# Performance work log

Hardware: AMD Instinct MI355X
Metric: run time of the kernel (lower is better)

The kernel has to match this reference:

```python
import jax, jax.numpy as jnp
import numpy as np

B, F, V, D_EMB = 16384, 32, 50000, 16
D_IN = F * D_EMB            # 512, concat embedding dim
N_TASK, N_SPEC, N_SH = 2, 2, 2
E = N_TASK * N_SPEC + N_SH  # 6 experts per CGC level
H1, H2 = 512, 256           # expert_params dims
T1, T2 = 128, 64            # tower dims


def setup_inputs() -> dict:
    key = jax.random.key(0)
    ks = iter(jax.random.split(key, 32))
    def w(shape, s=0.05):
        return jax.random.normal(next(ks), shape, jnp.float32) * s
    return dict(
        x_ids=jax.random.randint(next(ks), (B, F), 0, V),
        emb=w((F, V, D_EMB)),
        e1_W1=w((E, D_IN, H1)), e1_b1=jnp.zeros((E, H1), jnp.float32),
        e1_W2=w((E, H1, H2)), e1_b2=jnp.zeros((E, H2), jnp.float32),
        g1_Ws=w((N_TASK, D_IN, N_SPEC + N_SH)), g1_bs=jnp.zeros((N_TASK, N_SPEC + N_SH), jnp.float32),
        g1_Wsh=w((D_IN, E)), g1_bsh=jnp.zeros((E,), jnp.float32),
        e2_W1=w((E, H2, H1)), e2_b1=jnp.zeros((E, H1), jnp.float32),
        e2_W2=w((E, H1, H2)), e2_b2=jnp.zeros((E, H2), jnp.float32),
        g2_Ws=w((N_TASK, H2, N_SPEC + N_SH)), g2_bs=jnp.zeros((N_TASK, N_SPEC + N_SH), jnp.float32),
        tw_W1=w((N_TASK, H2, T1)), tw_b1=jnp.zeros((N_TASK, T1), jnp.float32),
        tw_W2=w((N_TASK, T1, T2)), tw_b2=jnp.zeros((N_TASK, T2), jnp.float32),
    )


def _cgc(x_list, W1, b1, W2, b2, Wg, bg, Wg_sh=None, bg_sh=None):
    # Stack expert inputs: task-t specific experts read x_list[t], shared read x_list[-1].
    X = jnp.stack([x_list[0]] * N_SPEC + [x_list[1]] * N_SPEC + [x_list[-1]] * N_SH)  # [E,B,Din]
    # Grouped two-layer expert MLP (BatchNorm is identity at eval-mode init).
    h = jax.nn.relu(jnp.einsum('ebd,edh->ebh', X, W1) + b1[:, None, :])   # [E,B,H1]
    out = jax.nn.relu(jnp.einsum('ebh,eho->ebo', h, W2) + b2[:, None, :])  # [E,B,H2]
    outs = []
    for t in range(N_TASK):
        gate = jax.nn.softmax(x_list[t] @ Wg[t] + bg[t], axis=-1)          # [B, N_SPEC+N_SH]
        sel = jnp.concatenate([out[t * N_SPEC:(t + 1) * N_SPEC], out[-N_SH:]], axis=0)
        outs.append(jnp.einsum('bk,kbo->bo', gate, sel))
    if Wg_sh is not None:  # shared gate only for levels < n_level
        gate = jax.nn.softmax(x_list[-1] @ Wg_sh + bg_sh, axis=-1)          # [B,E]
        outs.append(jnp.einsum('bk,kbo->bo', gate, out))
    return outs


def reference(x_ids, emb, e1_W1, e1_b1, e1_W2, e1_b2, g1_Ws, g1_bs, g1_Wsh, g1_bsh,
              e2_W1, e2_b1, e2_W2, e2_b2, g2_Ws, g2_bs, tw_W1, tw_b1, tw_W2, tw_b2):
    # Embedding lookup per sparse feature, then flatten (squeeze_dim=True).
    embed_x = emb[jnp.arange(F)[None, :], x_ids].reshape(B, D_IN)  # [B, 512]
    xs = [embed_x] * (N_TASK + 1)
    xs = _cgc(xs, e1_W1, e1_b1, e1_W2, e1_b2, g1_Ws, g1_bs, g1_Wsh, g1_bsh)  # level 1 -> 3 outs
    xs = _cgc(xs, e2_W1, e2_b1, e2_W2, e2_b2, g2_Ws, g2_bs)                  # level 2 -> 2 outs
    ys = []
    for t in range(N_TASK):
        h = jax.nn.relu(xs[t] @ tw_W1[t] + tw_b1[t])
        h = jax.nn.relu(h @ tw_W2[t] + tw_b2[t])
        ys.append(jax.nn.sigmoid(h))  # PredictionLayer('classification')
    return jnp.concatenate(ys, axis=1)  # [B, N_TASK*T2]
```

## Files before the change

kernel.cpp:

```cpp
#include <hip/hip_runtime.h>

typedef unsigned short u16;
typedef __attribute__((ext_vector_type(4))) unsigned short u16x4;
typedef __attribute__((ext_vector_type(8))) unsigned short u16x8;
typedef __attribute__((ext_vector_type(8))) short s16x8;
typedef __attribute__((ext_vector_type(4))) float f32x4;

#define BATCH 16384
#define NFEAT 32
#define NVOCAB 50000

__device__ __forceinline__ u16 f2bf(float f) {
    union { float f; unsigned u; } v; v.f = f;
    unsigned u = v.u;
    return (u16)((u + 0x7fffu + ((u >> 16) & 1u)) >> 16);
}
__device__ __forceinline__ float bf2f(u16 h) {
    union { unsigned u; float f; } v; v.u = ((unsigned)h) << 16;
    return v.f;
}

__device__ __forceinline__ void load_lds16(const u16* g, u16* l) {
    __builtin_amdgcn_global_load_lds(
        (const __attribute__((address_space(1))) void*)g,
        (__attribute__((address_space(3))) void*)l, 16, 0, 0);
}

struct PrepDesc { const float* src; u16* dst; int K; int N; int nz; int zbase; };
struct PrepArgs { PrepDesc d[6]; };

__global__ void prep_weights(PrepArgs args) {
    int z = blockIdx.z;
    int di = 0;
    #pragma unroll
    for (int i = 0; i < 6; i++)
        if (z >= args.d[i].zbase && z < args.d[i].zbase + args.d[i].nz) di = i;
    PrepDesc d = args.d[di];
    int zz = z - d.zbase;
    int k0 = blockIdx.x * 32, n0 = blockIdx.y * 32;
    if (k0 >= d.K || n0 >= d.N) return;
    __shared__ float tile[32][33];
    const float* src = d.src + (long)zz * d.K * d.N;
    u16* dst = d.dst + (long)zz * d.K * d.N;
    int tx = threadIdx.x & 31, ty = threadIdx.x >> 5;
    for (int r = ty; r < 32; r += 8) {
        int k = k0 + r, n = n0 + tx;
        tile[r][tx] = (k < d.K && n < d.N) ? src[(long)k * d.N + n] : 0.f;
    }
    __syncthreads();
    for (int r = ty; r < 32; r += 8) {
        int n = n0 + r, k = k0 + tx;
        if (n < d.N && k < d.K) dst[(long)n * d.K + k] = f2bf(tile[tx][r]);
    }
}

__global__ void gather_embed(const int* __restrict__ ids,
                             const float* __restrict__ emb,
                             u16* __restrict__ out) {
    int idx = blockIdx.x * 256 + threadIdx.x;
    int d4 = idx & 3;
    int f  = (idx >> 2) & 31;
    int b  = idx >> 7;
    int id = ids[b * NFEAT + f];
    const float4* p = (const float4*)(emb + ((long)f * NVOCAB + id) * 16) + d4;
    float4 v = *p;
    u16x4 o;
    o.x = f2bf(v.x); o.y = f2bf(v.y); o.z = f2bf(v.z); o.w = f2bf(v.w);
    *(u16x4*)(out + (long)b * 512 + f * 16 + d4 * 4) = o;
}

template<int ACT, typename OUT_T>
__global__ __launch_bounds__(256, 2)
void gemm_bt(const u16* __restrict__ A, const u16* __restrict__ Bt,
             const float* __restrict__ bias, OUT_T* __restrict__ C,
             int M, int N, int K,
             long a_zstride, int a_zdiv, long c_zstride, int c_row_stride) {
    __shared__ u16 sA[128 * 64];
    __shared__ u16 sB[128 * 64];
    const int z = blockIdx.z;
    const u16* Ab = A + (long)(z / a_zdiv) * a_zstride;
    const u16* Bb = Bt + (long)z * N * K;
    const int m0 = blockIdx.x * 128;
    const int n0 = blockIdx.y * 128;
    const int tid = threadIdx.x;
    const int lane = tid & 63;
    const int w = tid >> 6;
    const int wm = (w & 1) * 64;
    const int wn = (w >> 1) * 64;
    const int l16 = lane & 15;
    const int q = lane >> 4;

    const u16* gA[4];
    const u16* gB[4];
    u16* lA[4];
    u16* lB[4];
    #pragma unroll
    for (int i = 0; i < 4; i++) {
        int c = i * 256 + tid;
        int row = c >> 3;
        int lc = (c & 7) ^ (row & 7);
        gA[i] = Ab + (long)(m0 + row) * K + lc * 8;
        gB[i] = Bb + (long)(n0 + row) * K + lc * 8;
        int cb = (i * 256 + (tid & ~63)) * 8;
        lA[i] = &sA[cb];
        lB[i] = &sB[cb];
    }
    const int key = l16 & 7;

    f32x4 acc[4][4] = {};

    for (int k0 = 0; k0 < K; k0 += 64) {
        if (k0) __syncthreads();
        #pragma unroll
        for (int i = 0; i < 4; i++) load_lds16(gA[i] + k0, lA[i]);
        #pragma unroll
        for (int i = 0; i < 4; i++) load_lds16(gB[i] + k0, lB[i]);
        __syncthreads();
        #pragma unroll
        for (int kk = 0; kk < 2; kk++) {
            s16x8 af[4], bfr[4];
            #pragma unroll
            for (int i = 0; i < 4; i++) {
                int row = wm + i * 16 + l16;
                int pc = ((kk << 2) | q) ^ key;
                af[i] = *(const s16x8*)(&sA[row * 64 + pc * 8]);
            }
            #pragma unroll
            for (int i = 0; i < 4; i++) {
                int row = wn + i * 16 + l16;
                int pc = ((kk << 2) | q) ^ key;
                bfr[i] = *(const s16x8*)(&sB[row * 64 + pc * 8]);
            }
            #pragma unroll
            for (int mt = 0; mt < 4; mt++)
                #pragma unroll
                for (int nt = 0; nt < 4; nt++)
                    acc[mt][nt] = __builtin_amdgcn_mfma_f32_16x16x32_bf16(
                        bfr[nt], af[mt], acc[mt][nt], 0, 0, 0);
        }
    }

    const float* bb = bias + (long)z * N;
    OUT_T* Cp = C + (long)z * c_zstride;
    #pragma unroll
    for (int mt = 0; mt < 4; mt++) {
        int grow = m0 + wm + mt * 16 + l16;
        OUT_T* rowp = Cp + (long)grow * c_row_stride;
        #pragma unroll
        for (int nt = 0; nt < 4; nt++) {
            int gc = n0 + wn + nt * 16 + q * 4;
            if (gc >= N) continue;
            float4 bv = *(const float4*)(bb + gc);
            f32x4 v = acc[mt][nt];
            v.x += bv.x; v.y += bv.y; v.z += bv.z; v.w += bv.w;
            #pragma unroll
            for (int r = 0; r < 4; r++) {
                if (ACT == 1) v[r] = fmaxf(v[r], 0.f);
                else if (ACT == 2) v[r] = 1.f / (1.f + __expf(-v[r]));
            }
            if constexpr (sizeof(OUT_T) == 2) {
                u16x4 o;
                o.x = f2bf(v.x); o.y = f2bf(v.y); o.z = f2bf(v.z); o.w = f2bf(v.w);
                *(u16x4*)(rowp + gc) = o;
            } else {
                *(float4*)(rowp + gc) = *(float4*)&v;
            }
        }
    }
}

__global__ void gate_combine1(const u16* __restrict__ embed,
                              const u16* __restrict__ out1,
                              const float* __restrict__ g1Ws, const float* __restrict__ g1bs,
                              const float* __restrict__ gWsh, const float* __restrict__ gbsh,
                              u16* __restrict__ x1) {
    int b = blockIdx.x;
    __shared__ float sgw[14];
    int tid = threadIdx.x, w = tid >> 6, lane = tid & 63;
    if (w < 3) {
        int ng = (w == 2) ? 6 : 4;
        const float* W = (w == 2) ? gWsh : (g1Ws + w * 512 * 4);
        const u16* xr = embed + (long)b * 512;
        float lg[6] = {0, 0, 0, 0, 0, 0};
        for (int e = lane; e < 512; e += 64) {
            float xv = bf2f(xr[e]);
            #pragma unroll
            for (int g = 0; g < 6; g++)
                if (g < ng) lg[g] += xv * W[e * ng + g];
        }
        #pragma unroll
        for (int g = 0; g < 6; g++) {
            float v = lg[g];
            for (int off = 32; off > 0; off >>= 1) v += __shfl_xor(v, off);
            lg[g] = v;
        }
        if (lane == 0) {
            const float* bs = (w == 2) ? gbsh : (g1bs + w * 4);
            float mx = -1e30f;
            for (int g = 0; g < ng; g++) { lg[g] += bs[g]; mx = fmaxf(mx, lg[g]); }
            float s = 0.f, ex[6];
            for (int g = 0; g < ng; g++) { ex[g] = __expf(lg[g] - mx); s += ex[g]; }
            int base = (w == 2) ? 8 : w * 4;
            for (int g = 0; g < ng; g++) sgw[base + g] = ex[g] / s;
        }
    }
    __syncthreads();
    int j = tid;
    const u16* ob = out1 + (long)b * 256 + j;
    float o[6];
    #pragma unroll
    for (int k = 0; k < 6; k++) o[k] = bf2f(ob[(long)k * BATCH * 256]);
    float v0 = sgw[0] * o[0] + sgw[1] * o[1] + sgw[2] * o[4] + sgw[3] * o[5];
    float v1 = sgw[4] * o[2] + sgw[5] * o[3] + sgw[6] * o[4] + sgw[7] * o[5];
    float v2 = 0.f;
    #pragma unroll
    for (int k = 0; k < 6; k++) v2 += sgw[8 + k] * o[k];
    x1[((long)0 * BATCH + b) * 256 + j] = f2bf(v0);
    x1[((long)1 * BATCH + b) * 256 + j] = f2bf(v1);
    x1[((long)2 * BATCH + b) * 256 + j] = f2bf(v2);
}

__global__ void gate_combine2(const u16* __restrict__ x1,
                              const u16* __restrict__ out2,
                              const float* __restrict__ g2Ws, const float* __restrict__ g2bs,
                              u16* __restrict__ x2) {
    int b = blockIdx.x;
    __shared__ float sgw[8];
    int tid = threadIdx.x, w = tid >> 6, lane = tid & 63;
    if (w < 2) {
        const float* W = g2Ws + w * 256 * 4;
        const u16* xr = x1 + ((long)w * BATCH + b) * 256;
        float lg[4] = {0, 0, 0, 0};
        for (int e = lane; e < 256; e += 64) {
            float xv = bf2f(xr[e]);
            #pragma unroll
            for (int g = 0; g < 4; g++) lg[g] += xv * W[e * 4 + g];
        }
        #pragma unroll
        for (int g = 0; g < 4; g++) {
            float v = lg[g];
            for (int off = 32; off > 0; off >>= 1) v += __shfl_xor(v, off);
            lg[g] = v;
        }
        if (lane == 0) {
            float mx = -1e30f;
            for (int g = 0; g < 4; g++) { lg[g] += g2bs[w * 4 + g]; mx = fmaxf(mx, lg[g]); }
            float s = 0.f, ex[4];
            for (int g = 0; g < 4; g++) { ex[g] = __expf(lg[g] - mx); s += ex[g]; }
            for (int g = 0; g < 4; g++) sgw[w * 4 + g] = ex[g] / s;
        }
    }
    __syncthreads();
    int j = tid;
    const u16* ob = out2 + (long)b * 256 + j;
    float o[6];
    #pragma unroll
    for (int k = 0; k < 6; k++) o[k] = bf2f(ob[(long)k * BATCH * 256]);
    float v0 = sgw[0] * o[0] + sgw[1] * o[1] + sgw[2] * o[4] + sgw[3] * o[5];
    float v1 = sgw[4] * o[2] + sgw[5] * o[3] + sgw[6] * o[4] + sgw[7] * o[5];
    x2[((long)0 * BATCH + b) * 256 + j] = f2bf(v0);
    x2[((long)1 * BATCH + b) * 256 + j] = f2bf(v1);
}

extern "C" void kernel_launch(void* const* d_in, const int* in_sizes, int n_in,
                              void* d_out, int out_size, void* d_ws, size_t ws_size,
                              hipStream_t stream) {
    const int*   x_ids = (const int*)  d_in[0];
    const float* emb   = (const float*)d_in[1];
    const float* e1W1  = (const float*)d_in[2];
    const float* e1b1  = (const float*)d_in[3];
    const float* e1W2  = (const float*)d_in[4];
    const float* e1b2  = (const float*)d_in[5];
    const float* g1Ws  = (const float*)d_in[6];
    const float* g1bs  = (const float*)d_in[7];
    const float* g1Wsh = (const float*)d_in[8];
    const float* g1bsh = (const float*)d_in[9];
    const float* e2W1  = (const float*)d_in[10];
    const float* e2b1  = (const float*)d_in[11];
    const float* e2W2  = (const float*)d_in[12];
    const float* e2b2  = (const float*)d_in[13];
    const float* g2Ws  = (const float*)d_in[14];
    const float* g2bs  = (const float*)d_in[15];
    const float* twW1  = (const float*)d_in[16];
    const float* twb1  = (const float*)d_in[17];
    const float* twW2  = (const float*)d_in[18];
    const float* twb2  = (const float*)d_in[19];
    float* out = (float*)d_out;

    char* ws = (char*)d_ws;
    u16* embed   = (u16*)(ws + 0);
    u16* wt_e1W1 = (u16*)(ws + 16777216);
    u16* wt_e1W2 = (u16*)(ws + 19922944);
    u16* wt_e2W1 = (u16*)(ws + 21495808);
    u16* wt_e2W2 = (u16*)(ws + 23068672);
    u16* wt_twW1 = (u16*)(ws + 24641536);
    u16* wt_twW2 = (u16*)(ws + 24772608);
    u16* h_buf   = (u16*)(ws + 24805376);
    u16* o_buf   = (u16*)(ws + 125468672);
    u16* x1      = (u16*)(ws + 175800320);
    u16* x2      = (u16*)(ws + 200966144);
    u16* th      = (u16*)(ws + 217743360);

    PrepArgs pa;
    pa.d[0] = { e1W1, wt_e1W1, 512, 512, 6,  0 };
    pa.d[1] = { e1W2, wt_e1W2, 512, 256, 6,  6 };
    pa.d[2] = { e2W1, wt_e2W1, 256, 512, 6, 12 };
    pa.d[3] = { e2W2, wt_e2W2, 512, 256, 6, 18 };
    pa.d[4] = { twW1, wt_twW1, 256, 128, 2, 24 };
    pa.d[5] = { twW2, wt_twW2, 128,  64, 2, 26 };
    prep_weights<<<dim3(16, 16, 28), 256, 0, stream>>>(pa);

    gather_embed<<<dim3(BATCH * NFEAT * 4 / 256), 256, 0, stream>>>(x_ids, emb, embed);

    gemm_bt<1, u16><<<dim3(128, 4, 6), 256, 0, stream>>>(
        embed, wt_e1W1, e1b1, h_buf, BATCH, 512, 512,
        0L, 1, (long)BATCH * 512, 512);
    gemm_bt<1, u16><<<dim3(128, 2, 6), 256, 0, stream>>>(
        h_buf, wt_e1W2, e1b2, o_buf, BATCH, 256, 512,
        (long)BATCH * 512, 1, (long)BATCH * 256, 256);

    gate_combine1<<<dim3(BATCH), 256, 0, stream>>>(embed, o_buf, g1Ws, g1bs, g1Wsh, g1bsh, x1);

    gemm_bt<1, u16><<<dim3(128, 4, 6), 256, 0, stream>>>(
        x1, wt_e2W1, e2b1, h_buf, BATCH, 512, 256,
        (long)BATCH * 256, 2, (long)BATCH * 512, 512);
    gemm_bt<1, u16><<<dim3(128, 2, 6), 256, 0, stream>>>(
        h_buf, wt_e2W2, e2b2, o_buf, BATCH, 256, 512,
        (long)BATCH * 512, 1, (long)BATCH * 256, 256);

    gate_combine2<<<dim3(BATCH), 256, 0, stream>>>(x1, o_buf, g2Ws, g2bs, x2);

    gemm_bt<1, u16><<<dim3(128, 1, 2), 256, 0, stream>>>(
        x2, wt_twW1, twb1, th, BATCH, 128, 256,
        (long)BATCH * 256, 1, (long)BATCH * 128, 128);
    gemm_bt<2, float><<<dim3(128, 1, 2), 256, 0, stream>>>(
        th, wt_twW2, twb2, out, BATCH, 64, 128,
        (long)BATCH * 128, 1, 64L, 128);
}
```

Baseline: 534.1 us.

## Enlarge GEMM tiles, fuse tower MLP, and batch gate kernels over rows

Result: slower. 547.4 us (+2.5%).

```diff
diff --git a/kernel.cpp b/kernel.cpp
--- a/kernel.cpp
+++ b/kernel.cpp
@@ -69,197 +69,336 @@
     *(u16x4*)(out + (long)b * 512 + f * 16 + d4 * 4) = o;
 }
 
-template<int ACT, typename OUT_T>
-__global__ __launch_bounds__(256, 2)
-void gemm_bt(const u16* __restrict__ A, const u16* __restrict__ Bt,
-             const float* __restrict__ bias, OUT_T* __restrict__ C,
-             int M, int N, int K,
-             long a_zstride, int a_zdiv, long c_zstride, int c_row_stride) {
+struct GemmP {
+    const u16* A; const u16* Bt; const float* bias; u16* C;
+    int N, K, a_zshift, c_row_stride; long a_zstride, c_zstride;
+};
+
+__device__ __forceinline__ void gemm_impl(const GemmP p) {
     __shared__ u16 sA[128 * 64];
-    __shared__ u16 sB[128 * 64];
+    __shared__ u16 sB[256 * 64];
     const int z = blockIdx.z;
-    const u16* Ab = A + (long)(z / a_zdiv) * a_zstride;
-    const u16* Bb = Bt + (long)z * N * K;
+    const u16* Ab = p.A + (long)(z >> p.a_zshift) * p.a_zstride;
+    const u16* Bb = p.Bt + (long)z * p.N * p.K;
     const int m0 = blockIdx.x * 128;
-    const int n0 = blockIdx.y * 128;
+    const int n0 = blockIdx.y * 256;
     const int tid = threadIdx.x;
     const int lane = tid & 63;
     const int w = tid >> 6;
     const int wm = (w & 1) * 64;
-    const int wn = (w >> 1) * 64;
+    const int wn = (w >> 1) * 128;
     const int l16 = lane & 15;
     const int q = lane >> 4;
-
-    const u16* gA[4];
-    const u16* gB[4];
-    u16* lA[4];
-    u16* lB[4];
-    #pragma unroll
-    for (int i = 0; i < 4; i++) {
-        int c = i * 256 + tid;
-        int row = c >> 3;
-        int lc = (c & 7) ^ (row & 7);
-        gA[i] = Ab + (long)(m0 + row) * K + lc * 8;
-        gB[i] = Bb + (long)(n0 + row) * K + lc * 8;
-        int cb = (i * 256 + (tid & ~63)) * 8;
-        lA[i] = &sA[cb];
-        lB[i] = &sB[cb];
-    }
     const int key = l16 & 7;
-
-    f32x4 acc[4][4] = {};
+    const int K = p.K;
+
+    const int tr = tid >> 3;
+    const int lc = (tid & 7) ^ (tr & 7);
+    const u16* gA0 = Ab + (long)(m0 + tr) * K + lc * 8;
+    const u16* gB0 = Bb + (long)(n0 + tr) * K + lc * 8;
+    u16* lA0 = &sA[(tid & ~63) * 8];
+    u16* lB0 = &sB[(tid & ~63) * 8];
+
+    f32x4 acc[4][8] = {};
 
     for (int k0 = 0; k0 < K; k0 += 64) {
         if (k0) __syncthreads();
         #pragma unroll
-        for (int i = 0; i < 4; i++) load_lds16(gA[i] + k0, lA[i]);
-        #pragma unroll
-        for (int i = 0; i < 4; i++) load_lds16(gB[i] + k0, lB[i]);
+        for (int i = 0; i < 4; i++)
+            load_lds16(gA0 + (long)(32 * i) * K + k0, lA0 + i * 256 * 8);
+        #pragma unroll
+        for (int i = 0; i < 8; i++)
+            load_lds16(gB0 + (long)(32 * i) * K + k0, lB0 + i * 256 * 8);
         __syncthreads();
         #pragma unroll
         for (int kk = 0; kk < 2; kk++) {
-            s16x8 af[4], bfr[4];
+            const int pc = ((kk << 2) | q) ^ key;
+            s16x8 af[4], bf[8];
             #pragma unroll
-            for (int i = 0; i < 4; i++) {
-                int row = wm + i * 16 + l16;
-                int pc = ((kk << 2) | q) ^ key;
-                af[i] = *(const s16x8*)(&sA[row * 64 + pc * 8]);
-            }
+            for (int mt = 0; mt < 4; mt++)
+                af[mt] = *(const s16x8*)(&sA[(wm + mt * 16 + l16) * 64 + pc * 8]);
             #pragma unroll
-            for (int i = 0; i < 4; i++) {
-                int row = wn + i * 16 + l16;
-                int pc = ((kk << 2) | q) ^ key;
-                bfr[i] = *(const s16x8*)(&sB[row * 64 + pc * 8]);
-            }
+            for (int nt = 0; nt < 8; nt++)
+                bf[nt] = *(const s16x8*)(&sB[(wn + nt * 16 + l16) * 64 + pc * 8]);
             #pragma unroll
             for (int mt = 0; mt < 4; mt++)
                 #pragma unroll
-                for (int nt = 0; nt < 4; nt++)
+                for (int nt = 0; nt < 8; nt++)
                     acc[mt][nt] = __builtin_amdgcn_mfma_f32_16x16x32_bf16(
-                        bfr[nt], af[mt], acc[mt][nt], 0, 0, 0);
-        }
-    }
-
-    const float* bb = bias + (long)z * N;
-    OUT_T* Cp = C + (long)z * c_zstride;
+                        bf[nt], af[mt], acc[mt][nt], 0, 0, 0);
+        }
+    }
+
+    const float* bb = p.bias + (long)z * p.N;
+    u16* Cp = p.C + (long)z * p.c_zstride;
     #pragma unroll
     for (int mt = 0; mt < 4; mt++) {
         int grow = m0 + wm + mt * 16 + l16;
-        OUT_T* rowp = Cp + (long)grow * c_row_stride;
-        #pragma unroll
-        for (int nt = 0; nt < 4; nt++) {
+        u16* rowp = Cp + (long)grow * p.c_row_stride;
+        #pragma unroll
+        for (int nt = 0; nt < 8; nt++) {
             int gc = n0 + wn + nt * 16 + q * 4;
-            if (gc >= N) continue;
             float4 bv = *(const float4*)(bb + gc);
             f32x4 v = acc[mt][nt];
-            v.x += bv.x; v.y += bv.y; v.z += bv.z; v.w += bv.w;
+            v.x = fmaxf(v.x + bv.x, 0.f);
+            v.y = fmaxf(v.y + bv.y, 0.f);
+            v.z = fmaxf(v.z + bv.z, 0.f);
+            v.w = fmaxf(v.w + bv.w, 0.f);
+            u16x4 o;
+            o.x = f2bf(v.x); o.y = f2bf(v.y); o.z = f2bf(v.z); o.w = f2bf(v.w);
+            *(u16x4*)(rowp + gc) = o;
+        }
+    }
+}
+
+__global__ __launch_bounds__(256, 2) void gemm_l1a(GemmP p) { gemm_impl(p); }
+__global__ __launch_bounds__(256, 2) void gemm_l1b(GemmP p) { gemm_impl(p); }
+__global__ __launch_bounds__(256, 2) void gemm_l2a(GemmP p) { gemm_impl(p); }
+__global__ __launch_bounds__(256, 2) void gemm_l2b(GemmP p) { gemm_impl(p); }
+
+__global__ __launch_bounds__(256, 1)
+void tower_fused(const u16* __restrict__ x2, const u16* __restrict__ W1t,
+                 const float* __restrict__ b1, const u16* __restrict__ W2t,
+                 const float* __restrict__ b2, float* __restrict__ out) {
+    const int t = blockIdx.y, m0 = blockIdx.x * 64;
+    __shared__ u16 sX[64 * 256];
+    __shared__ u16 sW1[128 * 256];
+    __shared__ u16 sH[64 * 136];
+    __shared__ u16 sW2[64 * 128];
+    __shared__ float sB1[128];
+    __shared__ float sB2[64];
+    const int tid = threadIdx.x, lane = tid & 63, w = tid >> 6;
+    const int l16 = lane & 15, q = lane >> 4;
+
+    #pragma unroll
+    for (int i = 0; i < 8; i++) {
+        int c = i * 256 + tid, row = c >> 5, kc = c & 31;
+        int lcc = (kc & ~7) | ((kc & 7) ^ (row & 7));
+        load_lds16(x2 + ((long)t * BATCH + m0 + row) * 256 + lcc * 8,
+                   &sX[(i * 256 + (tid & ~63)) * 8]);
+    }
+    #pragma unroll
+    for (int i = 0; i < 16; i++) {
+        int c = i * 256 + tid, row = c >> 5, kc = c & 31;
+        int lcc = (kc & ~7) | ((kc & 7) ^ (row & 7));
+        load_lds16(W1t + ((long)t * 128 + row) * 256 + lcc * 8,
+                   &sW1[(i * 256 + (tid & ~63)) * 8]);
+    }
+    #pragma unroll
+    for (int i = 0; i < 4; i++) {
+        int c = i * 256 + tid, row = c >> 4, kc = c & 15;
+        int lcc = (kc & ~7) | ((kc & 7) ^ (row & 7));
+        load_lds16(W2t + ((long)t * 64 + row) * 128 + lcc * 8,
+                   &sW2[(i * 256 + (tid & ~63)) * 8]);
+    }
+    if (tid < 128) sB1[tid] = b1[t * 128 + tid];
+    if (tid < 64)  sB2[tid] = b2[t * 64 + tid];
+    __syncthreads();
+
+    f32x4 acc1[4][2] = {};
+    #pragma unroll
+    for (int kk = 0; kk < 8; kk++) {
+        int pcb = kk * 4 + q;
+        s16x8 af[4], bf[2];
+        #pragma unroll
+        for (int mt = 0; mt < 4; mt++) {
+            int row = mt * 16 + l16;
+            int sc = (pcb & ~7) | ((pcb & 7) ^ (row & 7));
+            af[mt] = *(const s16x8*)(&sX[row * 256 + sc * 8]);
+        }
+        #pragma unroll
+        for (int nt = 0; nt < 2; nt++) {
+            int row = w * 32 + nt * 16 + l16;
+            int sc = (pcb & ~7) | ((pcb & 7) ^ (row & 7));
+            bf[nt] = *(const s16x8*)(&sW1[row * 256 + sc * 8]);
+        }
+        #pragma unroll
+        for (int mt = 0; mt < 4; mt++)
             #pragma unroll
-            for (int r = 0; r < 4; r++) {
-                if (ACT == 1) v[r] = fmaxf(v[r], 0.f);
-                else if (ACT == 2) v[r] = 1.f / (1.f + __expf(-v[r]));
-            }
-            if constexpr (sizeof(OUT_T) == 2) {
-                u16x4 o;
-                o.x = f2bf(v.x); o.y = f2bf(v.y); o.z = f2bf(v.z); o.w = f2bf(v.w);
-                *(u16x4*)(rowp + gc) = o;
-            } else {
-                *(float4*)(rowp + gc) = *(float4*)&v;
-            }
-        }
-    }
-}
-
-__global__ void gate_combine1(const u16* __restrict__ embed,
-                              const u16* __restrict__ out1,
-                              const float* __restrict__ g1Ws, const float* __restrict__ g1bs,
-                              const float* __restrict__ gWsh, const float* __restrict__ gbsh,
-                              u16* __restrict__ x1) {
-    int b = blockIdx.x;
-    __shared__ float sgw[14];
-    int tid = threadIdx.x, w = tid >> 6, lane = tid & 63;
-    if (w < 3) {
-        int ng = (w == 2) ? 6 : 4;
-        const float* W = (w == 2) ? gWsh : (g1Ws + w * 512 * 4);
-        const u16* xr = embed + (long)b * 512;
-        float lg[6] = {0, 0, 0, 0, 0, 0};
-        for (int e = lane; e < 512; e += 64) {
-            float xv = bf2f(xr[e]);
+            for (int nt = 0; nt < 2; nt++)
+                acc1[mt][nt] = __builtin_amdgcn_mfma_f32_16x16x32_bf16(
+                    bf[nt], af[mt], acc1[mt][nt], 0, 0, 0);
+    }
+    #pragma unroll
+    for (int mt = 0; mt < 4; mt++) {
+        int row = mt * 16 + l16;
+        #pragma unroll
+        for (int nt = 0; nt < 2; nt++) {
+            int col = w * 32 + nt * 16 + q * 4;
+            f32x4 v = acc1[mt][nt];
+            u16x4 o;
+            o.x = f2bf(fmaxf(v.x + sB1[col + 0], 0.f));
+            o.y = f2bf(fmaxf(v.y + sB1[col + 1], 0.f));
+            o.z = f2bf(fmaxf(v.z + sB1[col + 2], 0.f));
+            o.w = f2bf(fmaxf(v.w + sB1[col + 3], 0.f));
+            *(u16x4*)(&sH[row * 136 + col]) = o;
+        }
+    }
+    __syncthreads();
+
+    f32x4 acc2[4] = {};
+    #pragma unroll
+    for (int kk = 0; kk < 4; kk++) {
+        s16x8 af[4], bf;
+        #pragma unroll
+        for (int mt = 0; mt < 4; mt++) {
+            int row = mt * 16 + l16;
+            af[mt] = *(const s16x8*)(&sH[row * 136 + kk * 32 + q * 8]);
+        }
+        {
+            int row = w * 16 + l16;
+            int pc = kk * 4 + q;
+            int sc = (pc & ~7) | ((pc & 7) ^ (row & 7));
+            bf = *(const s16x8*)(&sW2[row * 128 + sc * 8]);
+        }
+        #pragma unroll
+        for (int mt = 0; mt < 4; mt++)
+            acc2[mt] = __builtin_amdgcn_mfma_f32_16x16x32_bf16(
+                bf, af[mt], acc2[mt], 0, 0, 0);
+    }
+    #pragma unroll
+    for (int mt = 0; mt < 4; mt++) {
+        int grow = m0 + mt * 16 + l16;
+        int col = w * 16 + q * 4;
+        float4 bv = *(const float4*)(sB2 + col);
+        f32x4 v = acc2[mt];
+        float4 r;
+        r.x = 1.f / (1.f + __expf(-(v.x + bv.x)));
+        r.y = 1.f / (1.f + __expf(-(v.y + bv.y)));
+        r.z = 1.f / (1.f + __expf(-(v.z + bv.z)));
+        r.w = 1.f / (1.f + __expf(-(v.w + bv.w)));
+        *(float4*)(out + (long)grow * 128 + t * 64 + col) = r;
+    }
+}
+
+__global__ __launch_bounds__(256)
+void gate1(const u16* __restrict__ embed, const u16* __restrict__ out1,
+           const float* __restrict__ g1Ws, const float* __restrict__ g1bs,
+           const float* __restrict__ gWsh, const float* __restrict__ gbsh,
+           u16* __restrict__ x1) {
+    const int m0 = blockIdx.x * 64;
+    __shared__ float sg[64][16];
+    const int tid = threadIdx.x;
+    const int row = tid >> 2, pp = tid & 3;
+
+    float a[4] = {0, 0, 0, 0}, b[4] = {0, 0, 0, 0}, c[6] = {0, 0, 0, 0, 0, 0};
+    const u16* er = embed + (long)(m0 + row) * 512 + pp * 128;
+    const float* Wa = g1Ws;
+    const float* Wb = g1Ws + 2048;
+    for (int j = 0; j < 128; j += 8) {
+        u16x8 xv8 = *(const u16x8*)(er + j);
+        #pragma unroll
+        for (int u = 0; u < 8; u++) {
+            float xv = bf2f(xv8[u]);
+            int k = pp * 128 + j + u;
+            float4 wa = *(const float4*)(Wa + k * 4);
+            float4 wb = *(const float4*)(Wb + k * 4);
+            a[0] += xv * wa.x; a[1] += xv * wa.y; a[2] += xv * wa.z; a[3] += xv * wa.w;
+            b[0] += xv * wb.x; b[1] += xv * wb.y; b[2] += xv * wb.z; b[3] += xv * wb.w;
+            const float* wc = gWsh + k * 6;
             #pragma unroll
-            for (int g = 0; g < 6; g++)
-                if (g < ng) lg[g] += xv * W[e * ng + g];
-        }
-        #pragma unroll
-        for (int g = 0; g < 6; g++) {
-            float v = lg[g];
-            for (int off = 32; off > 0; off >>= 1) v += __shfl_xor(v, off);
-            lg[g] = v;
-        }
-        if (lane == 0) {
-            const float* bs = (w == 2) ? gbsh : (g1bs + w * 4);
-            float mx = -1e30f;
-            for (int g = 0; g < ng; g++) { lg[g] += bs[g]; mx = fmaxf(mx, lg[g]); }
-            float s = 0.f, ex[6];
-            for (int g = 0; g < ng; g++) { ex[g] = __expf(lg[g] - mx); s += ex[g]; }
-            int base = (w == 2) ? 8 : w * 4;
-            for (int g = 0; g < ng; g++) sgw[base + g] = ex[g] / s;
-        }
+            for (int g = 0; g < 6; g++) c[g] += xv * wc[g];
+        }
+    }
+    #pragma unroll
+    for (int g = 0; g < 4; g++) {
+        a[g] += __shfl_xor(a[g], 1); a[g] += __shfl_xor(a[g], 2);
+        b[g] += __shfl_xor(b[g], 1); b[g] += __shfl_xor(b[g], 2);
+    }
+    #pragma unroll
+    for (int g = 0; g < 6; g++) { c[g] += __shfl_xor(c[g], 1); c[g] += __shfl_xor(c[g], 2); }
+    if (pp == 0) {
+        float mx, s, e[6];
+        mx = -1e30f;
+        for (int g = 0; g < 4; g++) { a[g] += g1bs[g]; mx = fmaxf(mx, a[g]); }
+        s = 0.f; for (int g = 0; g < 4; g++) { e[g] = __expf(a[g] - mx); s += e[g]; }
+        for (int g = 0; g < 4; g++) sg[row][g] = e[g] / s;
+        mx = -1e30f;
+        for (int g = 0; g < 4; g++) { b[g] += g1bs[4 + g]; mx = fmaxf(mx, b[g]); }
+        s = 0.f; for (int g = 0; g < 4; g++) { e[g] = __expf(b[g] - mx); s += e[g]; }
+        for (int g = 0; g < 4; g++) sg[row][4 + g] = e[g] / s;
+        mx = -1e30f;
+        for (int g = 0; g < 6; g++) { c[g] += gbsh[g]; mx = fmaxf(mx, c[g]); }
+        s = 0.f; for (int g = 0; g < 6; g++) { e[g] = __expf(c[g] - mx); s += e[g]; }
+        for (int g = 0; g < 6; g++) sg[row][8 + g] = e[g] / s;
     }
     __syncthreads();
-    int j = tid;
-    const u16* ob = out1 + (long)b * 256 + j;
-    float o[6];
-    #pragma unroll
-    for (int k = 0; k < 6; k++) o[k] = bf2f(ob[(long)k * BATCH * 256]);
-    float v0 = sgw[0] * o[0] + sgw[1] * o[1] + sgw[2] * o[4] + sgw[3] * o[5];
-    float v1 = sgw[4] * o[2] + sgw[5] * o[3] + sgw[6] * o[4] + sgw[7] * o[5];
-    float v2 = 0.f;
-    #pragma unroll
-    for (int k = 0; k < 6; k++) v2 += sgw[8 + k] * o[k];
-    x1[((long)0 * BATCH + b) * 256 + j] = f2bf(v0);
-    x1[((long)1 * BATCH + b) * 256 + j] = f2bf(v1);
-    x1[((long)2 * BATCH + b) * 256 + j] = f2bf(v2);
-}
-
-__global__ void gate_combine2(const u16* __restrict__ x1,
-                              const u16* __restrict__ out2,
-                              const float* __restrict__ g2Ws, const float* __restrict__ g2bs,
-                              u16* __restrict__ x2) {
-    int b = blockIdx.x;
-    __shared__ float sgw[8];
-    int tid = threadIdx.x, w = tid >> 6, lane = tid & 63;
-    if (w < 2) {
-        const float* W = g2Ws + w * 256 * 4;
-        const u16* xr = x1 + ((long)w * BATCH + b) * 256;
-        float lg[4] = {0, 0, 0, 0};
-        for (int e = lane; e < 256; e += 64) {
-            float xv = bf2f(xr[e]);
-            #pragma unroll
-            for (int g = 0; g < 4; g++) lg[g] += xv * W[e * 4 + g];
-        }
-        #pragma unroll
-        for (int g = 0; g < 4; g++) {
-            float v = lg[g];
-            for (int off = 32; off > 0; off >>= 1) v += __shfl_xor(v, off);
-            lg[g] = v;
-        }
-        if (lane == 0) {
-            float mx = -1e30f;
-            for (int g = 0; g < 4; g++) { lg[g] += g2bs[w * 4 + g]; mx = fmaxf(mx, lg[g]); }
-            float s = 0.f, ex[4];
-            for (int g = 0; g < 4; g++) { ex[g] = __expf(lg[g] - mx); s += ex[g]; }
-            for (int g = 0; g < 4; g++) sgw[w * 4 + g] = ex[g] / s;
-        }
+
+    for (int r = 0; r < 64; r++) {
+        long rb = m0 + r;
+        float o[6];
+        #pragma unroll
+        for (int k = 0; k < 6; k++)
+            o[k] = bf2f(out1[((long)k * BATCH + rb) * 256 + tid]);
+        const float* g = sg[r];
+        float v0 = g[0] * o[0] + g[1] * o[1] + g[2] * o[4] + g[3] * o[5];
+        float v1 = g[4] * o[2] + g[5] * o[3] + g[6] * o[4] + g[7] * o[5];
+        float v2 = 0.f;
+        #pragma unroll
+        for (int k = 0; k < 6; k++) v2 += g[8 + k] * o[k];
+        x1[((long)0 * BATCH + rb) * 256 + tid] = f2bf(v0);
+        x1[((long)1 * BATCH + rb) * 256 + tid] = f2bf(v1);
+        x1[((long)2 * BATCH + rb) * 256 + tid] = f2bf(v2);
+    }
+}
+
+__global__ __launch_bounds__(256)
+void gate2(const u16* __restrict__ x1, const u16* __restrict__ out2,
+           const float* __restrict__ g2Ws, const float* __restrict__ g2bs,
+           u16* __restrict__ x2) {
+    const int m0 = blockIdx.x * 64;
+    __shared__ float sg[64][8];
+    const int tid = threadIdx.x;
+    const int row = tid >> 2, pp = tid & 3;
+
+    float a[4] = {0, 0, 0, 0}, b[4] = {0, 0, 0, 0};
+    const u16* e0 = x1 + ((long)0 * BATCH + m0 + row) * 256 + pp * 64;
+    const u16* e1 = x1 + ((long)1 * BATCH + m0 + row) * 256 + pp * 64;
+    const float* Wa = g2Ws;
+    const float* Wb = g2Ws + 1024;
+    for (int j = 0; j < 64; j += 8) {
+        u16x8 x0 = *(const u16x8*)(e0 + j);
+        u16x8 x1v = *(const u16x8*)(e1 + j);
+        #pragma unroll
+        for (int u = 0; u < 8; u++) {
+            int k = pp * 64 + j + u;
+            float4 wa = *(const float4*)(Wa + k * 4);
+            float4 wb = *(const float4*)(Wb + k * 4);
+            float xv0 = bf2f(x0[u]), xv1 = bf2f(x1v[u]);
+            a[0] += xv0 * wa.x; a[1] += xv0 * wa.y; a[2] += xv0 * wa.z; a[3] += xv0 * wa.w;
+            b[0] += xv1 * wb.x; b[1] += xv1 * wb.y; b[2] += xv1 * wb.z; b[3] += xv1 * wb.w;
+        }
+    }
+    #pragma unroll
+    for (int g = 0; g < 4; g++) {
+        a[g] += __shfl_xor(a[g], 1); a[g] += __shfl_xor(a[g], 2);
+        b[g] += __shfl_xor(b[g], 1); b[g] += __shfl_xor(b[g], 2);
+    }
+    if (pp == 0) {
+        float mx, s, e[4];
+        mx = -1e30f;
+        for (int g = 0; g < 4; g++) { a[g] += g2bs[g]; mx = fmaxf(mx, a[g]); }
+        s = 0.f; for (int g = 0; g < 4; g++) { e[g] = __expf(a[g] - mx); s += e[g]; }
+        for (int g = 0; g < 4; g++) sg[row][g] = e[g] / s;
+        mx = -1e30f;
+        for (int g = 0; g < 4; g++) { b[g] += g2bs[4 + g]; mx = fmaxf(mx, b[g]); }
+        s = 0.f; for (int g = 0; g < 4; g++) { e[g] = __expf(b[g] - mx); s += e[g]; }
+        for (int g = 0; g < 4; g++) sg[row][4 + g] = e[g] / s;
     }
     __syncthreads();
-    int j = tid;
-    const u16* ob = out2 + (long)b * 256 + j;
-    float o[6];
-    #pragma unroll
-    for (int k = 0; k < 6; k++) o[k] = bf2f(ob[(long)k * BATCH * 256]);
-    float v0 = sgw[0] * o[0] + sgw[1] * o[1] + sgw[2] * o[4] + sgw[3] * o[5];
-    float v1 = sgw[4] * o[2] + sgw[5] * o[3] + sgw[6] * o[4] + sgw[7] * o[5];
-    x2[((long)0 * BATCH + b) * 256 + j] = f2bf(v0);
-    x2[((long)1 * BATCH + b) * 256 + j] = f2bf(v1);
+
+    for (int r = 0; r < 64; r++) {
+        long rb = m0 + r;
+        float o[6];
+        #pragma unroll
+        for (int k = 0; k < 6; k++)
+            o[k] = bf2f(out2[((long)k * BATCH + rb) * 256 + tid]);
+        const float* g = sg[r];
+        float v0 = g[0] * o[0] + g[1] * o[1] + g[2] * o[4] + g[3] * o[5];
+        float v1 = g[4] * o[2] + g[5] * o[3] + g[6] * o[4] + g[7] * o[5];
+        x2[((long)0 * BATCH + rb) * 256 + tid] = f2bf(v0);
+        x2[((long)1 * BATCH + rb) * 256 + tid] = f2bf(v1);
+    }
 }
 
 extern "C" void kernel_launch(void* const* d_in, const int* in_sizes, int n_in,
@@ -299,7 +438,6 @@
     u16* o_buf   = (u16*)(ws + 125468672);
     u16* x1      = (u16*)(ws + 175800320);
     u16* x2      = (u16*)(ws + 200966144);
-    u16* th      = (u16*)(ws + 217743360);
 
     PrepArgs pa;
     pa.d[0] = { e1W1, wt_e1W1, 512, 512, 6,  0 };
@@ -312,28 +450,24 @@
 
     gather_embed<<<dim3(BATCH * NFEAT * 4 / 256), 256, 0, stream>>>(x_ids, emb, embed);
 
-    gemm_bt<1, u16><<<dim3(128, 4, 6), 256, 0, stream>>>(
-        embed, wt_e1W1, e1b1, h_buf, BATCH, 512, 512,
-        0L, 1, (long)BATCH * 512, 512);
-    gemm_bt<1, u16><<<dim3(128, 2, 6), 256, 0, stream>>>(
-        h_buf, wt_e1W2, e1b2, o_buf, BATCH, 256, 512,
-        (long)BATCH * 512, 1, (long)BATCH * 256, 256);
-
-    gate_combine1<<<dim3(BATCH), 256, 0, stream>>>(embed, o_buf, g1Ws, g1bs, g1Wsh, g1bsh, x1);
-
-    gemm_bt<1, u16><<<dim3(128, 4, 6), 256, 0, stream>>>(
-        x1, wt_e2W1, e2b1, h_buf, BATCH, 512, 256,
-        (long)BATCH * 256, 2, (long)BATCH * 512, 512);
-    gemm_bt<1, u16><<<dim3(128, 2, 6), 256, 0, stream>>>(
-        h_buf, wt_e2W2, e2b2, o_buf, BATCH, 256, 512,
-        (long)BATCH * 512, 1, (long)BATCH * 256, 256);
-
-    gate_combine2<<<dim3(BATCH), 256, 0, stream>>>(x1, o_buf, g2Ws, g2bs, x2);
-
-    gemm_bt<1, u16><<<dim3(128, 1, 2), 256, 0, stream>>>(
-        x2, wt_twW1, twb1, th, BATCH, 128, 256,
-        (long)BATCH * 256, 1, (long)BATCH * 128, 128);
-    gemm_bt<2, float><<<dim3(128, 1, 2), 256, 0, stream>>>(
-        th, wt_twW2, twb2, out, BATCH, 64, 128,
-        (long)BATCH * 128, 1, 64L, 128);
-}
+    GemmP p1a = { embed, wt_e1W1, e1b1, h_buf, 512, 512, 0, 512, 0L, (long)BATCH * 512 };
+    gemm_l1a<<<dim3(128, 2, 6), 256, 0, stream>>>(p1a);
+
+    GemmP p1b = { h_buf, wt_e1W2, e1b2, o_buf, 256, 512, 0, 256,
+                  (long)BATCH * 512, (long)BATCH * 256 };
+    gemm_l1b<<<dim3(128, 1, 6), 256, 0, stream>>>(p1b);
+
+    gate1<<<dim3(BATCH / 64), 256, 0, stream>>>(embed, o_buf, g1Ws, g1bs, g1Wsh, g1bsh, x1);
+
+    GemmP p2a = { x1, wt_e2W1, e2b1, h_buf, 512, 256, 1, 512,
+                  (long)BATCH * 256, (long)BATCH * 512 };
+    gemm_l2a<<<dim3(128, 2, 6), 256, 0, stream>>>(p2a);
+
+    GemmP p2b = { h_buf, wt_e2W2, e2b2, o_buf, 256, 512, 0, 256,
+                  (long)BATCH * 512, (long)BATCH * 256 };
+    gemm_l2b<<<dim3(128, 1, 6), 256, 0, stream>>>(p2b);
+
+    gate2<<<dim3(BATCH / 64), 256, 0, stream>>>(x1, o_buf, g2Ws, g2bs, x2);
+
+    tower_fused<<<dim3(BATCH / 64, 2), 256, 0, stream>>>(x2, wt_twW1, twb1, wt_twW2, twb2, out);
+}
```
